# Kernel optimization log

Hardware: AMD Instinct MI355X
Metric: run time of the kernel (lower is better)

## Reference

```python
import jax, jax.numpy as jnp
import numpy as np

N_NODES = 50000
N_EDGES = 800000
F_IN, D1, N_CLS = 128, 128, 64


def gcn_conv(x, W, b, src, dst, n):
    # x: [N, Fin] -> linear transform then normalized scatter-add aggregation
    h = x @ W  # [N, Fout]
    deg = jnp.zeros((n,), h.dtype).at[dst].add(jnp.ones((dst.shape[0],), h.dtype))
    dis = jnp.where(deg > 0, jax.lax.rsqrt(jnp.maximum(deg, 1.0)), 0.0)  # deg^-1/2, inf->0
    norm = dis[src] * dis[dst]  # [E_tot]
    msgs = norm[:, None] * h[src]  # gather source features, scale by sym norm
    out = jax.ops.segment_sum(msgs, dst, num_segments=n)  # scatter-add to targets
    return out + b


def setup_inputs() -> dict:
    key = jax.random.key(0)
    ks = jax.random.split(key, 6)
    x = jax.random.normal(ks[0], (N_NODES, F_IN), dtype=jnp.float32)
    edge_index = jax.random.randint(ks[1], (2, N_EDGES), 0, N_NODES, dtype=jnp.int64)
    W1 = jax.random.normal(ks[2], (F_IN, D1), dtype=jnp.float32) / np.sqrt(F_IN)
    b1 = jnp.zeros((D1,), dtype=jnp.float32)
    W2 = jax.random.normal(ks[3], (D1, N_CLS), dtype=jnp.float32) / np.sqrt(D1)
    b2 = jnp.zeros((N_CLS,), dtype=jnp.float32)
    return {"x": x, "edge_index": edge_index, "W1": W1, "b1": b1, "W2": W2, "b2": b2}


def reference(x, edge_index, W1, b1, W2, b2):
    n = x.shape[0]
    loops = jnp.arange(n, dtype=edge_index.dtype)
    src = jnp.concatenate([edge_index[0], loops])  # add self-loops (PyG default)
    dst = jnp.concatenate([edge_index[1], loops])
    h = gcn_conv(x, W1, b1, src, dst, n)
    h = jax.nn.relu(h)
    # F.dropout(training=self.training) is identity in eval mode
    out = gcn_conv(h, W2, b2, src, dst, n)
    return out
```

## Files before the change

### kernel.cpp

```cpp
#include <hip/hip_runtime.h>

#define NN 50000
#define NE 800000
#define CAP 64
#define NPAD 50176
#define SLICE 6250

typedef unsigned int   u32;
typedef unsigned short u16;
typedef __attribute__((ext_vector_type(8))) short short8;
typedef __attribute__((ext_vector_type(4))) float f32x4;

__device__ inline u16 f2bf(float f) {
    u32 u = __float_as_uint(f);
    return (u16)((u + 0x7FFF + ((u >> 16) & 1)) >> 16);
}
__device__ inline float bfval(u16 h) { return __uint_as_float(((u32)h) << 16); }
__device__ inline float bf_lo(u32 u) { return __uint_as_float(u << 16); }
__device__ inline float bf_hi(u32 u) { return __uint_as_float(u & 0xFFFF0000u); }


__global__ __launch_bounds__(256) void build_ell(const int* __restrict__ ei,
                                                 int* __restrict__ cnt,
                                                 u16* __restrict__ ell) {
    const int s  = blockIdx.x & 7;
    const int g  = blockIdx.x >> 3;
    const int ng = gridDim.x >> 3;
    const int lo = s * SLICE, hi = lo + SLICE;
    for (int e0 = (g * 256 + (int)threadIdx.x) * 4; e0 < NE; e0 += ng * 1024) {
        int4 d4 = *(const int4*)(ei + NE + e0);
        int dv[4] = {d4.x, d4.y, d4.z, d4.w};
#pragma unroll
        for (int k = 0; k < 4; ++k) {
            int d = dv[k];
            if (d >= lo && d < hi) {
                int src = ei[e0 + k];
                int sh = k & 1;
                int pos = atomicAdd(&cnt[sh * NPAD + d], 1);
                if (pos < 32) ell[d * CAP + sh * 32 + pos] = (u16)src;
            }
        }
    }
}


__global__ __launch_bounds__(256) void prep_w(const float* __restrict__ W1,
                                              const float* __restrict__ W2,
                                              u16* __restrict__ W1h, u16* __restrict__ W1l,
                                              u16* __restrict__ W2h, u16* __restrict__ W2l,
                                              int* __restrict__ cnt) {
    int i = blockIdx.x * 256 + threadIdx.x;
    for (int z = i; z < 2 * NPAD; z += 32768) cnt[z] = 0;
    const float* W; u16 *Dh, *Dl; int NOUT, idx;
    if (i < 16384) { W = W1; Dh = W1h; Dl = W1l; NOUT = 128; idx = i; }
    else           { idx = i - 16384; if (idx >= 8192) return;
                     W = W2; Dh = W2h; Dl = W2l; NOUT = 64; }
    int j = idx & 7, l = (idx >> 3) & 63, kc = (idx >> 9) & 3, t = idx >> 11;
    int k = kc * 32 + (l >> 4) * 8 + j;
    int n = t * 16 + (l & 15);
    float w = W[k * NOUT + n];
    u16 h = f2bf(w);
    Dh[idx] = h;
    Dl[idx] = f2bf(w - bfval(h));
}


template <int NOUT>
__global__ __launch_bounds__(256) void gemm_mfma(const float* __restrict__ A,
                                                 const u16* __restrict__ Wh,
                                                 const u16* __restrict__ Wl,
                                                 u16* __restrict__ C, int M) {
    constexpr int NT = NOUT / 16;
    const int tid = threadIdx.x;
    const int w = tid >> 6, l = tid & 63;
    const int m = l & 15, q = l >> 4;

    int arow = blockIdx.x * 64 + w * 16 + m;
    const float* Ar = A + (size_t)min(arow, M - 1) * 128;

    f32x4 acc[NT] = {};

#pragma unroll
    for (int kc = 0; kc < 4; ++kc) {
        float p[8];
        *(float4*)&p[0] = *(const float4*)(Ar + kc * 32 + q * 8);
        *(float4*)&p[4] = *(const float4*)(Ar + kc * 32 + q * 8 + 4);
        short8 ah, al;
#pragma unroll
        for (int j = 0; j < 8; ++j) {
            u16 h = f2bf(p[j]);
            ah[j] = (short)h;
            al[j] = (short)f2bf(p[j] - bfval(h));
        }
#pragma unroll
        for (int t = 0; t < NT; ++t) {
            size_t bo = ((size_t)(t * 4 + kc) * 64 + l) * 8;
            short8 bh = *(const short8*)(Wh + bo);
            short8 bl = *(const short8*)(Wl + bo);
            acc[t] = __builtin_amdgcn_mfma_f32_16x16x32_bf16(ah, bh, acc[t], 0, 0, 0);
            acc[t] = __builtin_amdgcn_mfma_f32_16x16x32_bf16(al, bh, acc[t], 0, 0, 0);
            acc[t] = __builtin_amdgcn_mfma_f32_16x16x32_bf16(ah, bl, acc[t], 0, 0, 0);
        }
    }

    int growbase = blockIdx.x * 64 + w * 16 + q * 4;
#pragma unroll
    for (int t = 0; t < NT; ++t)
#pragma unroll
        for (int r = 0; r < 4; ++r) {
            int grow = growbase + r;
            if (grow < M) C[(size_t)grow * NOUT + t * 16 + m] = f2bf(acc[t][r]);
        }
}


__global__ __launch_bounds__(256) void gemm_mfma_bf(const u16* __restrict__ A,
                                                    const u16* __restrict__ Wh,
                                                    const u16* __restrict__ Wl,
                                                    u16* __restrict__ C, int M) {
    constexpr int NT = 4;
    const int tid = threadIdx.x;
    const int w = tid >> 6, l = tid & 63;
    const int m = l & 15, q = l >> 4;

    int arow = blockIdx.x * 64 + w * 16 + m;
    const u16* Ar = A + (size_t)min(arow, M - 1) * 128;

    f32x4 acc[NT] = {};

#pragma unroll
    for (int kc = 0; kc < 4; ++kc) {
        short8 ah = *(const short8*)(Ar + kc * 32 + q * 8);
#pragma unroll
        for (int t = 0; t < NT; ++t) {
            size_t bo = ((size_t)(t * 4 + kc) * 64 + l) * 8;
            short8 bh = *(const short8*)(Wh + bo);
            short8 bl = *(const short8*)(Wl + bo);
            acc[t] = __builtin_amdgcn_mfma_f32_16x16x32_bf16(ah, bh, acc[t], 0, 0, 0);
            acc[t] = __builtin_amdgcn_mfma_f32_16x16x32_bf16(ah, bl, acc[t], 0, 0, 0);
        }
    }

    int growbase = blockIdx.x * 64 + w * 16 + q * 4;
#pragma unroll
    for (int t = 0; t < NT; ++t)
#pragma unroll
        for (int r = 0; r < 4; ++r) {
            int grow = growbase + r;
            if (grow < M) C[(size_t)grow * 64 + t * 16 + m] = f2bf(acc[t][r]);
        }
}


template <int F, bool RELU, bool OUTBF>
__global__ __launch_bounds__(256) void aggregate(const u16* __restrict__ H,
                                                 const u16* __restrict__ ell,
                                                 const int* __restrict__ cnt,
                                                 const float* __restrict__ bias,
                                                 void* __restrict__ outp) {
    const int tid = threadIdx.x;
    const int node = (int)((blockIdx.x * 256 + tid) >> 6);
    if (node >= NN) return;
    const int lane = tid & 63;

    const int c0r = cnt[node], c1r = cnt[NPAD + node];
    const int c0 = min(c0r, 32), c1 = min(c1r, 32);
    const int ne = min(c0 + c1, 63);
    const float di = rsqrtf((float)(c0r + c1r + 1));
    int slot = (lane < c0) ? lane : 32 + (lane - c0);
    int   s_l = (lane < ne) ? (int)ell[(size_t)node * CAP + slot] : node;
    float n_l = (lane <= ne)
                    ? rsqrtf((float)(cnt[s_l] + cnt[NPAD + s_l] + 1)) * di
                    : 0.0f;

    constexpr int G = (F == 128) ? 4 : 8;
    constexpr int L = 64 / G;
    const int g = lane / L;
    const int ci = lane & (L - 1);

    const int m = ne + 1;
    const int mPad = (m + 2 * G - 1) & ~(2 * G - 1);

    float acc[8] = {0, 0, 0, 0, 0, 0, 0, 0};
    for (int j = 0; j < mPad; j += 2 * G) {
        int   sA = __shfl(s_l, j + g);
        float nA = __shfl(n_l, j + g);
        int   sB = __shfl(s_l, j + G + g);
        float nB = __shfl(n_l, j + G + g);
        uint4 vA = *(const uint4*)(H + (size_t)sA * F + ci * 8);
        uint4 vB = *(const uint4*)(H + (size_t)sB * F + ci * 8);
        acc[0] += nA * bf_lo(vA.x); acc[1] += nA * bf_hi(vA.x);
        acc[2] += nA * bf_lo(vA.y); acc[3] += nA * bf_hi(vA.y);
        acc[4] += nA * bf_lo(vA.z); acc[5] += nA * bf_hi(vA.z);
        acc[6] += nA * bf_lo(vA.w); acc[7] += nA * bf_hi(vA.w);
        acc[0] += nB * bf_lo(vB.x); acc[1] += nB * bf_hi(vB.x);
        acc[2] += nB * bf_lo(vB.y); acc[3] += nB * bf_hi(vB.y);
        acc[4] += nB * bf_lo(vB.z); acc[5] += nB * bf_hi(vB.z);
        acc[6] += nB * bf_lo(vB.w); acc[7] += nB * bf_hi(vB.w);
    }

#pragma unroll
    for (int i = 0; i < 8; ++i) {
        if (F == 64) acc[i] += __shfl_xor(acc[i], 8);
        acc[i] += __shfl_xor(acc[i], 16);
        acc[i] += __shfl_xor(acc[i], 32);
    }

    const int active = (F == 128) ? 32 : 16;
    if (lane < active) {
        int part, c0i;
        if (F == 128) { part = lane >> 4;       c0i = (lane & 15) * 8 + part * 4; }
        else          { part = (lane >> 3) & 1; c0i = (lane & 7) * 8 + part * 4; }
        float4 b4 = *(const float4*)(bias + c0i);
        float4 o = make_float4(acc[part * 4 + 0] + b4.x, acc[part * 4 + 1] + b4.y,
                               acc[part * 4 + 2] + b4.z, acc[part * 4 + 3] + b4.w);
        if (RELU) { o.x = fmaxf(o.x, 0.f); o.y = fmaxf(o.y, 0.f);
                    o.z = fmaxf(o.z, 0.f); o.w = fmaxf(o.w, 0.f); }
        if (OUTBF) {
            u16* out = (u16*)outp;
            *(ushort4*)(out + (size_t)node * F + c0i) =
                make_ushort4(f2bf(o.x), f2bf(o.y), f2bf(o.z), f2bf(o.w));
        } else {
            float* out = (float*)outp;
            *(float4*)(out + (size_t)node * F + c0i) = o;
        }
    }
}


extern "C" void kernel_launch(void* const* d_in, const int* in_sizes, int n_in,
                              void* d_out, int out_size, void* d_ws, size_t ws_size,
                              hipStream_t stream) {
    const float* x  = (const float*)d_in[0];
    const int*   ei = (const int*)d_in[1];
    const float* W1 = (const float*)d_in[2];
    const float* b1 = (const float*)d_in[3];
    const float* W2 = (const float*)d_in[4];
    const float* b2 = (const float*)d_in[5];
    float* out = (float*)d_out;

    char* ws = (char*)d_ws;
    size_t off = 0;
    int* cnt = (int*)ws;                     off += (size_t)2 * NPAD * 4;
    u16* ell = (u16*)(ws + off);             off += (size_t)NN * CAP * 2;
    off = (off + 255) & ~(size_t)255;
    u16* W1h = (u16*)(ws + off);             off += 16384 * 2;
    u16* W1l = (u16*)(ws + off);             off += 16384 * 2;
    u16* W2h = (u16*)(ws + off);             off += 8192 * 2;
    u16* W2l = (u16*)(ws + off);             off += 8192 * 2;
    off = (off + 255) & ~(size_t)255;
    u16* Hbf = (u16*)(ws + off);             off += (size_t)NN * 128 * 2;
    u16* Abf = (u16*)(ws + off);             off += (size_t)NN * 128 * 2;

    prep_w<<<128, 256, 0, stream>>>(W1, W2, W1h, W1l, W2h, W2l, cnt);
    build_ell<<<1600, 256, 0, stream>>>(ei, cnt, ell);

    gemm_mfma<128><<<(NN + 63) / 64, 256, 0, stream>>>(x, W1h, W1l, Hbf, NN);
    aggregate<128, true, true><<<(NN + 3) / 4, 256, 0, stream>>>(Hbf, ell, cnt, b1, Abf);

    gemm_mfma_bf<<<(NN + 63) / 64, 256, 0, stream>>>(Abf, W2h, W2l, Hbf, NN);
    aggregate<64, false, false><<<(NN + 3) / 4, 256, 0, stream>>>(Hbf, ell, cnt, b2, out);
}
```

Measured before the change: 198.8 us.

## Chunk features into 32-column slabs and precompute per-edge norms for aggregation

Feature matrices are stored as column chunks of 32 bf16 (chunk-major), and aggregation is split into one block per chunk per 4 nodes. Each chunk's gathered working set is smaller, which is meant to raise cache locality for the random neighbor gathers. A new build_norm kernel precomputes neighbor indices, symmetric norms and edge counts once, reusing a compact u16 degree table written in the first GEMM. Both layers then reuse these arrays. The cost is an extra kernel, extra workspace traffic, and re-reading the neighbor and norm lists once per chunk.

Result: slower. 245.6 us (+23.5%).

```diff
diff --git a/kernel.cpp b/kernel.cpp
--- a/kernel.cpp
+++ b/kernel.cpp
@@ -69,9 +69,17 @@
 __global__ __launch_bounds__(256) void gemm_mfma(const float* __restrict__ A,
                                                  const u16* __restrict__ Wh,
                                                  const u16* __restrict__ Wl,
-                                                 u16* __restrict__ C, int M) {
+                                                 u16* __restrict__ C, int M,
+                                                 const int* __restrict__ cnt,
+                                                 u16* __restrict__ degT) {
     constexpr int NT = NOUT / 16;
     const int tid = threadIdx.x;
+
+    if (tid < 64) {
+        int node = blockIdx.x * 64 + tid;
+        if (node < NN) degT[node] = (u16)(cnt[node] + cnt[NPAD + node] + 1);
+    }
+
     const int w = tid >> 6, l = tid & 63;
     const int m = l & 15, q = l >> 4;
 
@@ -109,7 +117,9 @@
 #pragma unroll
         for (int r = 0; r < 4; ++r) {
             int grow = growbase + r;
-            if (grow < M) C[(size_t)grow * NOUT + t * 16 + m] = f2bf(acc[t][r]);
+            if (grow < M)
+                C[(size_t)(t >> 1) * NN * 32 + (size_t)grow * 32 + (t & 1) * 16 + m] =
+                    f2bf(acc[t][r]);
         }
 }
 
@@ -124,13 +134,13 @@
     const int m = l & 15, q = l >> 4;
 
     int arow = blockIdx.x * 64 + w * 16 + m;
-    const u16* Ar = A + (size_t)min(arow, M - 1) * 128;
+    const size_t ar = (size_t)min(arow, M - 1) * 32;
 
     f32x4 acc[NT] = {};
 
 #pragma unroll
     for (int kc = 0; kc < 4; ++kc) {
-        short8 ah = *(const short8*)(Ar + kc * 32 + q * 8);
+        short8 ah = *(const short8*)(A + (size_t)kc * NN * 32 + ar + q * 8);
 #pragma unroll
         for (int t = 0; t < NT; ++t) {
             size_t bo = ((size_t)(t * 4 + kc) * 64 + l) * 8;
@@ -147,17 +157,19 @@
 #pragma unroll
         for (int r = 0; r < 4; ++r) {
             int grow = growbase + r;
-            if (grow < M) C[(size_t)grow * 64 + t * 16 + m] = f2bf(acc[t][r]);
-        }
-}
-
-
-template <int F, bool RELU, bool OUTBF>
-__global__ __launch_bounds__(256) void aggregate(const u16* __restrict__ H,
-                                                 const u16* __restrict__ ell,
-                                                 const int* __restrict__ cnt,
-                                                 const float* __restrict__ bias,
-                                                 void* __restrict__ outp) {
+            if (grow < M)
+                C[(size_t)(t >> 1) * NN * 32 + (size_t)grow * 32 + (t & 1) * 16 + m] =
+                    f2bf(acc[t][r]);
+        }
+}
+
+
+__global__ __launch_bounds__(256) void build_norm(const int* __restrict__ cnt,
+                                                  const u16* __restrict__ ell,
+                                                  const u16* __restrict__ degT,
+                                                  u16* __restrict__ els,
+                                                  float* __restrict__ nrm,
+                                                  int* __restrict__ mArr) {
     const int tid = threadIdx.x;
     const int node = (int)((blockIdx.x * 256 + tid) >> 6);
     if (node >= NN) return;
@@ -169,60 +181,70 @@
     const float di = rsqrtf((float)(c0r + c1r + 1));
     int slot = (lane < c0) ? lane : 32 + (lane - c0);
     int   s_l = (lane < ne) ? (int)ell[(size_t)node * CAP + slot] : node;
-    float n_l = (lane <= ne)
-                    ? rsqrtf((float)(cnt[s_l] + cnt[NPAD + s_l] + 1)) * di
-                    : 0.0f;
-
-    constexpr int G = (F == 128) ? 4 : 8;
-    constexpr int L = 64 / G;
-    const int g = lane / L;
-    const int ci = lane & (L - 1);
-
-    const int m = ne + 1;
-    const int mPad = (m + 2 * G - 1) & ~(2 * G - 1);
-
-    float acc[8] = {0, 0, 0, 0, 0, 0, 0, 0};
-    for (int j = 0; j < mPad; j += 2 * G) {
+    float n_l = (lane <= ne) ? rsqrtf((float)degT[s_l]) * di : 0.0f;
+
+    els[(size_t)node * 64 + lane] = (u16)s_l;
+    nrm[(size_t)node * 64 + lane] = n_l;
+    if (lane == 0) mArr[node] = ne + 1;
+}
+
+
+template <int NCH, bool RELU, bool OUTBF>
+__global__ __launch_bounds__(256) void aggregate_ch(const u16* __restrict__ H,
+                                                    const u16* __restrict__ els,
+                                                    const float* __restrict__ nrm,
+                                                    const int* __restrict__ mArr,
+                                                    const float* __restrict__ bias,
+                                                    void* __restrict__ outp) {
+    constexpr int NB = (NN + 3) / 4;
+    const int tid = threadIdx.x;
+    const int chunk = blockIdx.x / NB;
+    const int nb = blockIdx.x - chunk * NB;
+    const int node = nb * 4 + (tid >> 6);
+    if (node >= NN) return;
+    const int lane = tid & 63;
+    const int g = lane >> 3, ci = lane & 7;
+
+    const int m = mArr[node];
+    const int mPad = (m + 15) & ~15;
+    int   s_l = (int)els[(size_t)node * 64 + lane];
+    float n_l = nrm[(size_t)node * 64 + lane];
+
+    const u16* Hc = H + (size_t)chunk * NN * 32;
+    float acc[4] = {0, 0, 0, 0};
+    for (int j = 0; j < mPad; j += 16) {
         int   sA = __shfl(s_l, j + g);
         float nA = __shfl(n_l, j + g);
-        int   sB = __shfl(s_l, j + G + g);
-        float nB = __shfl(n_l, j + G + g);
-        uint4 vA = *(const uint4*)(H + (size_t)sA * F + ci * 8);
-        uint4 vB = *(const uint4*)(H + (size_t)sB * F + ci * 8);
+        int   sB = __shfl(s_l, j + 8 + g);
+        float nB = __shfl(n_l, j + 8 + g);
+        uint2 vA = *(const uint2*)(Hc + (size_t)sA * 32 + ci * 4);
+        uint2 vB = *(const uint2*)(Hc + (size_t)sB * 32 + ci * 4);
         acc[0] += nA * bf_lo(vA.x); acc[1] += nA * bf_hi(vA.x);
         acc[2] += nA * bf_lo(vA.y); acc[3] += nA * bf_hi(vA.y);
-        acc[4] += nA * bf_lo(vA.z); acc[5] += nA * bf_hi(vA.z);
-        acc[6] += nA * bf_lo(vA.w); acc[7] += nA * bf_hi(vA.w);
         acc[0] += nB * bf_lo(vB.x); acc[1] += nB * bf_hi(vB.x);
         acc[2] += nB * bf_lo(vB.y); acc[3] += nB * bf_hi(vB.y);
-        acc[4] += nB * bf_lo(vB.z); acc[5] += nB * bf_hi(vB.z);
-        acc[6] += nB * bf_lo(vB.w); acc[7] += nB * bf_hi(vB.w);
-    }
-
-#pragma unroll
-    for (int i = 0; i < 8; ++i) {
-        if (F == 64) acc[i] += __shfl_xor(acc[i], 8);
+    }
+
+#pragma unroll
+    for (int i = 0; i < 4; ++i) {
+        acc[i] += __shfl_xor(acc[i], 8);
         acc[i] += __shfl_xor(acc[i], 16);
         acc[i] += __shfl_xor(acc[i], 32);
     }
 
-    const int active = (F == 128) ? 32 : 16;
-    if (lane < active) {
-        int part, c0i;
-        if (F == 128) { part = lane >> 4;       c0i = (lane & 15) * 8 + part * 4; }
-        else          { part = (lane >> 3) & 1; c0i = (lane & 7) * 8 + part * 4; }
-        float4 b4 = *(const float4*)(bias + c0i);
-        float4 o = make_float4(acc[part * 4 + 0] + b4.x, acc[part * 4 + 1] + b4.y,
-                               acc[part * 4 + 2] + b4.z, acc[part * 4 + 3] + b4.w);
+    if (lane < 8) {
+        float4 b4 = *(const float4*)(bias + chunk * 32 + lane * 4);
+        float4 o = make_float4(acc[0] + b4.x, acc[1] + b4.y,
+                               acc[2] + b4.z, acc[3] + b4.w);
         if (RELU) { o.x = fmaxf(o.x, 0.f); o.y = fmaxf(o.y, 0.f);
                     o.z = fmaxf(o.z, 0.f); o.w = fmaxf(o.w, 0.f); }
         if (OUTBF) {
             u16* out = (u16*)outp;
-            *(ushort4*)(out + (size_t)node * F + c0i) =
+            *(ushort4*)(out + (size_t)chunk * NN * 32 + (size_t)node * 32 + lane * 4) =
                 make_ushort4(f2bf(o.x), f2bf(o.y), f2bf(o.z), f2bf(o.w));
         } else {
             float* out = (float*)outp;
-            *(float4*)(out + (size_t)node * F + c0i) = o;
+            *(float4*)(out + (size_t)node * (NCH * 32) + chunk * 32 + lane * 4) = o;
         }
     }
 }
@@ -249,15 +271,23 @@
     u16* W2h = (u16*)(ws + off);             off += 8192 * 2;
     u16* W2l = (u16*)(ws + off);             off += 8192 * 2;
     off = (off + 255) & ~(size_t)255;
+    u16* els = (u16*)(ws + off);             off += (size_t)NN * 64 * 2;
+    float* nrm = (float*)(ws + off);         off += (size_t)NN * 64 * 4;
+    int* mArr = (int*)(ws + off);            off += (size_t)NN * 4;
+    u16* degT = (u16*)(ws + off);            off += (size_t)NN * 2;
+    off = (off + 255) & ~(size_t)255;
     u16* Hbf = (u16*)(ws + off);             off += (size_t)NN * 128 * 2;
     u16* Abf = (u16*)(ws + off);             off += (size_t)NN * 128 * 2;
 
     prep_w<<<128, 256, 0, stream>>>(W1, W2, W1h, W1l, W2h, W2l, cnt);
     build_ell<<<1600, 256, 0, stream>>>(ei, cnt, ell);
 
-    gemm_mfma<128><<<(NN + 63) / 64, 256, 0, stream>>>(x, W1h, W1l, Hbf, NN);
-    aggregate<128, true, true><<<(NN + 3) / 4, 256, 0, stream>>>(Hbf, ell, cnt, b1, Abf);
+    gemm_mfma<128><<<(NN + 63) / 64, 256, 0, stream>>>(x, W1h, W1l, Hbf, NN, cnt, degT);
+    build_norm<<<(NN + 3) / 4, 256, 0, stream>>>(cnt, ell, degT, els, nrm, mArr);
+    aggregate_ch<4, true, true><<<4 * ((NN + 3) / 4), 256, 0, stream>>>(
+        Hbf, els, nrm, mArr, b1, Abf);
 
     gemm_mfma_bf<<<(NN + 63) / 64, 256, 0, stream>>>(Abf, W2h, W2l, Hbf, NN);
-    aggregate<64, false, false><<<(NN + 3) / 4, 256, 0, stream>>>(Hbf, ell, cnt, b2, out);
-}
+    aggregate_ch<2, false, false><<<2 * ((NN + 3) / 4), 256, 0, stream>>>(
+        Hbf, els, nrm, mArr, b2, out);
+}
```

## Precompute degree table, persistent aggregation with prefetch and simpler reduction layout

Applied to the files above, without the earlier changes.

The first GEMM now also writes a compact u16 degree table, so aggregation reads one small value per neighbour instead of two int counts. Aggregation becomes a grid-stride persistent kernel over 2048 blocks. It walks neighbours in groups with a one-step software prefetch of the next feature row, and each lane owns 8 contiguous output columns so stores are wider. Layer 2 features go to a separate buffer. The aim is to cut gather latency and metadata traffic, at the cost of less memory-level parallelism per iteration than the old two-load unrolled loop.

Measured after the change: 197.3 us. No clear change (-0.8%).

```diff
diff --git a/kernel.cpp b/kernel.cpp
--- a/kernel.cpp
+++ b/kernel.cpp
@@ -65,13 +65,20 @@
 }
 
 
-template <int NOUT>
-__global__ __launch_bounds__(256) void gemm_mfma(const float* __restrict__ A,
-                                                 const u16* __restrict__ Wh,
-                                                 const u16* __restrict__ Wl,
-                                                 u16* __restrict__ C, int M) {
-    constexpr int NT = NOUT / 16;
+__global__ __launch_bounds__(256) void gemm_mfma1(const float* __restrict__ A,
+                                                  const u16* __restrict__ Wh,
+                                                  const u16* __restrict__ Wl,
+                                                  u16* __restrict__ C, int M,
+                                                  const int* __restrict__ cnt,
+                                                  u16* __restrict__ degT) {
+    constexpr int NT = 8;
     const int tid = threadIdx.x;
+
+    if (tid < 64) {
+        int node = blockIdx.x * 64 + tid;
+        if (node < NN) degT[node] = (u16)(cnt[node] + cnt[NPAD + node] + 1);
+    }
+
     const int w = tid >> 6, l = tid & 63;
     const int m = l & 15, q = l >> 4;
 
@@ -109,7 +116,7 @@
 #pragma unroll
         for (int r = 0; r < 4; ++r) {
             int grow = growbase + r;
-            if (grow < M) C[(size_t)grow * NOUT + t * 16 + m] = f2bf(acc[t][r]);
+            if (grow < M) C[(size_t)grow * 128 + t * 16 + m] = f2bf(acc[t][r]);
         }
 }
 
@@ -153,76 +160,77 @@
 
 
 template <int F, bool RELU, bool OUTBF>
-__global__ __launch_bounds__(256) void aggregate(const u16* __restrict__ H,
-                                                 const u16* __restrict__ ell,
-                                                 const int* __restrict__ cnt,
-                                                 const float* __restrict__ bias,
-                                                 void* __restrict__ outp) {
+__global__ __launch_bounds__(256) void aggregate_bf(const u16* __restrict__ H,
+                                                    const u16* __restrict__ ell,
+                                                    const int* __restrict__ cnt,
+                                                    const u16* __restrict__ degT,
+                                                    const float* __restrict__ bias,
+                                                    void* __restrict__ outp) {
     const int tid = threadIdx.x;
-    const int node = (int)((blockIdx.x * 256 + tid) >> 6);
-    if (node >= NN) return;
     const int lane = tid & 63;
-
-    const int c0r = cnt[node], c1r = cnt[NPAD + node];
-    const int c0 = min(c0r, 32), c1 = min(c1r, 32);
-    const int ne = min(c0 + c1, 63);
-    const float di = rsqrtf((float)(c0r + c1r + 1));
-    int slot = (lane < c0) ? lane : 32 + (lane - c0);
-    int   s_l = (lane < ne) ? (int)ell[(size_t)node * CAP + slot] : node;
-    float n_l = (lane <= ne)
-                    ? rsqrtf((float)(cnt[s_l] + cnt[NPAD + s_l] + 1)) * di
-                    : 0.0f;
-
-    constexpr int G = (F == 128) ? 4 : 8;
-    constexpr int L = 64 / G;
+    const int wid = (int)((blockIdx.x * 256 + tid) >> 6);
+    const int nw = (int)((gridDim.x * 256) >> 6);
+
+    constexpr int L = F / 8;
+    constexpr int G = 64 / L;
     const int g = lane / L;
     const int ci = lane & (L - 1);
 
-    const int m = ne + 1;
-    const int mPad = (m + 2 * G - 1) & ~(2 * G - 1);
-
-    float acc[8] = {0, 0, 0, 0, 0, 0, 0, 0};
-    for (int j = 0; j < mPad; j += 2 * G) {
-        int   sA = __shfl(s_l, j + g);
-        float nA = __shfl(n_l, j + g);
-        int   sB = __shfl(s_l, j + G + g);
-        float nB = __shfl(n_l, j + G + g);
-        uint4 vA = *(const uint4*)(H + (size_t)sA * F + ci * 8);
-        uint4 vB = *(const uint4*)(H + (size_t)sB * F + ci * 8);
-        acc[0] += nA * bf_lo(vA.x); acc[1] += nA * bf_hi(vA.x);
-        acc[2] += nA * bf_lo(vA.y); acc[3] += nA * bf_hi(vA.y);
-        acc[4] += nA * bf_lo(vA.z); acc[5] += nA * bf_hi(vA.z);
-        acc[6] += nA * bf_lo(vA.w); acc[7] += nA * bf_hi(vA.w);
-        acc[0] += nB * bf_lo(vB.x); acc[1] += nB * bf_hi(vB.x);
-        acc[2] += nB * bf_lo(vB.y); acc[3] += nB * bf_hi(vB.y);
-        acc[4] += nB * bf_lo(vB.z); acc[5] += nB * bf_hi(vB.z);
-        acc[6] += nB * bf_lo(vB.w); acc[7] += nB * bf_hi(vB.w);
-    }
-
-#pragma unroll
-    for (int i = 0; i < 8; ++i) {
-        if (F == 64) acc[i] += __shfl_xor(acc[i], 8);
-        acc[i] += __shfl_xor(acc[i], 16);
-        acc[i] += __shfl_xor(acc[i], 32);
-    }
-
-    const int active = (F == 128) ? 32 : 16;
-    if (lane < active) {
-        int part, c0i;
-        if (F == 128) { part = lane >> 4;       c0i = (lane & 15) * 8 + part * 4; }
-        else          { part = (lane >> 3) & 1; c0i = (lane & 7) * 8 + part * 4; }
-        float4 b4 = *(const float4*)(bias + c0i);
-        float4 o = make_float4(acc[part * 4 + 0] + b4.x, acc[part * 4 + 1] + b4.y,
-                               acc[part * 4 + 2] + b4.z, acc[part * 4 + 3] + b4.w);
-        if (RELU) { o.x = fmaxf(o.x, 0.f); o.y = fmaxf(o.y, 0.f);
-                    o.z = fmaxf(o.z, 0.f); o.w = fmaxf(o.w, 0.f); }
-        if (OUTBF) {
-            u16* out = (u16*)outp;
-            *(ushort4*)(out + (size_t)node * F + c0i) =
-                make_ushort4(f2bf(o.x), f2bf(o.y), f2bf(o.z), f2bf(o.w));
-        } else {
-            float* out = (float*)outp;
-            *(float4*)(out + (size_t)node * F + c0i) = o;
+    for (int node = wid; node < NN; node += nw) {
+        const int c0r = cnt[node], c1r = cnt[NPAD + node];
+        const int c0 = min(c0r, 32), c1 = min(c1r, 32);
+        const int ne = min(c0 + c1, 63);
+        const float di = rsqrtf((float)(c0r + c1r + 1));
+        int slot = (lane < c0) ? lane : 32 + (lane - c0);
+        int   s_l = (lane < ne) ? (int)ell[(size_t)node * CAP + slot] : node;
+        float n_l = (lane <= ne) ? rsqrtf((float)degT[s_l]) * di : 0.0f;
+
+        const int ng = (ne + G) / G;
+
+        int   sC = __shfl(s_l, g);
+        float nC = __shfl(n_l, g);
+        uint4 vC = *(const uint4*)(H + (size_t)sC * F + ci * 8);
+
+        float acc[8] = {0, 0, 0, 0, 0, 0, 0, 0};
+        for (int gi = 0; gi < ng; ++gi) {
+            int gn = min(gi + 1, ng - 1);
+            int   sN = __shfl(s_l, gn * G + g);
+            float nN = __shfl(n_l, gn * G + g);
+            uint4 vN = *(const uint4*)(H + (size_t)sN * F + ci * 8);
+            acc[0] += nC * bf_lo(vC.x); acc[1] += nC * bf_hi(vC.x);
+            acc[2] += nC * bf_lo(vC.y); acc[3] += nC * bf_hi(vC.y);
+            acc[4] += nC * bf_lo(vC.z); acc[5] += nC * bf_hi(vC.z);
+            acc[6] += nC * bf_lo(vC.w); acc[7] += nC * bf_hi(vC.w);
+            vC = vN;
+            nC = (gi + 1 < ng) ? nN : 0.0f;
+        }
+
+#pragma unroll
+        for (int i = 0; i < 8; ++i) {
+            if (L <= 8) acc[i] += __shfl_xor(acc[i], 8);
+            acc[i] += __shfl_xor(acc[i], 16);
+            acc[i] += __shfl_xor(acc[i], 32);
+        }
+
+        if (lane < L) {
+            float4 b0 = *(const float4*)(bias + lane * 8);
+            float4 b1 = *(const float4*)(bias + lane * 8 + 4);
+            float o[8] = {acc[0] + b0.x, acc[1] + b0.y, acc[2] + b0.z,
+                          acc[3] + b0.w, acc[4] + b1.x, acc[5] + b1.y,
+                          acc[6] + b1.z, acc[7] + b1.w};
+            if (RELU)
+#pragma unroll
+                for (int k = 0; k < 8; ++k) o[k] = fmaxf(o[k], 0.f);
+            if (OUTBF) {
+                union { ushort4 s4[2]; uint4 q; } pk;
+                pk.s4[0] = make_ushort4(f2bf(o[0]), f2bf(o[1]), f2bf(o[2]), f2bf(o[3]));
+                pk.s4[1] = make_ushort4(f2bf(o[4]), f2bf(o[5]), f2bf(o[6]), f2bf(o[7]));
+                *(uint4*)((u16*)outp + (size_t)node * F + lane * 8) = pk.q;
+            } else {
+                float* out = (float*)outp + (size_t)node * F + lane * 8;
+                *(float4*)out = make_float4(o[0], o[1], o[2], o[3]);
+                *(float4*)(out + 4) = make_float4(o[4], o[5], o[6], o[7]);
+            }
         }
     }
 }
@@ -249,15 +257,20 @@
     u16* W2h = (u16*)(ws + off);             off += 8192 * 2;
     u16* W2l = (u16*)(ws + off);             off += 8192 * 2;
     off = (off + 255) & ~(size_t)255;
+    u16* degT = (u16*)(ws + off);            off += (size_t)NPAD * 2;
+    off = (off + 255) & ~(size_t)255;
     u16* Hbf = (u16*)(ws + off);             off += (size_t)NN * 128 * 2;
     u16* Abf = (u16*)(ws + off);             off += (size_t)NN * 128 * 2;
+    u16* H2b = (u16*)(ws + off);             off += (size_t)NN * 64 * 2;
 
     prep_w<<<128, 256, 0, stream>>>(W1, W2, W1h, W1l, W2h, W2l, cnt);
     build_ell<<<1600, 256, 0, stream>>>(ei, cnt, ell);
 
-    gemm_mfma<128><<<(NN + 63) / 64, 256, 0, stream>>>(x, W1h, W1l, Hbf, NN);
-    aggregate<128, true, true><<<(NN + 3) / 4, 256, 0, stream>>>(Hbf, ell, cnt, b1, Abf);
-
-    gemm_mfma_bf<<<(NN + 63) / 64, 256, 0, stream>>>(Abf, W2h, W2l, Hbf, NN);
-    aggregate<64, false, false><<<(NN + 3) / 4, 256, 0, stream>>>(Hbf, ell, cnt, b2, out);
-}
+    gemm_mfma1<<<(NN + 63) / 64, 256, 0, stream>>>(x, W1h, W1l, Hbf, NN, cnt, degT);
+    aggregate_bf<128, true, true><<<2048, 256, 0, stream>>>(
+        Hbf, ell, cnt, degT, b1, Abf);
+
+    gemm_mfma_bf<<<(NN + 63) / 64, 256, 0, stream>>>(Abf, W2h, W2l, H2b, NN);
+    aggregate_bf<64, false, false><<<2048, 256, 0, stream>>>(
+        H2b, ell, cnt, degT, b2, out);
+}
```
